# Kernel tuning notes

Hardware: AMD Instinct MI355X
Metric: run time of the kernel (lower is better)

Reference implementation:

```python
import jax, jax.numpy as jnp
import numpy as np

DELTA = 2.5749
BN_EPS = 1e-5
N_LAYERS = 5


def _gin_pna_conv(x, src, dst, nW1, nb1, nW2, nb2, mW, mb):
    # x: [N, D]; src/dst: [E]
    N = x.shape[0]
    msgs = x[src]                                   # [E, D] gather (message = x_j)
    cnt = jax.ops.segment_sum(jnp.ones_like(dst, dtype=x.dtype), dst, num_segments=N)  # [N]
    c = jnp.maximum(cnt, 1.0)[:, None]              # guard isolated nodes
    sums = jax.ops.segment_sum(msgs, dst, num_segments=N)          # [N, D]
    maxs = jax.ops.segment_max(msgs, dst, num_segments=N)
    maxs = jnp.where(cnt[:, None] > 0, maxs, 0.0)   # empty segments -> 0 (torch_scatter behavior)
    means = sums / c
    sq_means = jax.ops.segment_sum(msgs * msgs, dst, num_segments=N) / c
    var = jax.nn.relu(sq_means - means * means)
    base = jnp.concatenate([sums, maxs, means, var], axis=1)        # [N, 4D]
    amp = (c / DELTA) * base                        # amplification scaler
    att = (DELTA / c) * base                        # attenuation scaler
    comb = jnp.concatenate([base, amp, att], axis=1)                # [N, 12D]
    agg = comb @ mW.T + mb                          # mlp: 12D -> D
    h = agg + x                                     # GIN: (1+eps)*x_r + aggr, eps=0
    h = jax.nn.relu(h @ nW1.T + nb1) @ nW2.T + nb2  # nn = Linear-ReLU-Linear
    return h


def _batchnorm(x, gamma, beta):
    mu = jnp.mean(x, axis=0)
    var = jnp.var(x, axis=0)
    return (x - mu) * jax.lax.rsqrt(var + BN_EPS) * gamma + beta


def setup_inputs() -> dict:
    key = jax.random.key(0)
    ks = jax.random.split(key, 12)
    N, E, D, G, OUT = 100000, 1600000, 64, 512, 16
    s = 0.05
    p = lambda k, shape: jax.random.normal(k, shape, dtype=jnp.float32) * s
    return {
        "x": jax.random.normal(ks[0], (N, D), dtype=jnp.float32),
        "edge_index": jax.random.randint(ks[1], (2, E), 0, N),
        "batch": jnp.sort(jax.random.randint(ks[2], (N,), 0, G)),
        "encW": p(ks[3], (D, D)), "encb": jnp.zeros((D,), jnp.float32),
        "nnW1": p(ks[4], (N_LAYERS, D, D)), "nnb1": jnp.zeros((N_LAYERS, D), jnp.float32),
        "nnW2": p(ks[5], (N_LAYERS, D, D)), "nnb2": jnp.zeros((N_LAYERS, D), jnp.float32),
        "mlpW": p(ks[6], (N_LAYERS, D, 12 * D)), "mlpb": jnp.zeros((N_LAYERS, D), jnp.float32),
        "bnG": jnp.ones((N_LAYERS, D), jnp.float32), "bnB": jnp.zeros((N_LAYERS, D), jnp.float32),
        "fc1W": p(ks[7], (D, D)), "fc1b": jnp.zeros((D,), jnp.float32),
        "fc2W": p(ks[8], (OUT, D)), "fc2b": jnp.zeros((OUT,), jnp.float32),
    }


def reference(x, edge_index, batch, encW, encb, nnW1, nnb1, nnW2, nnb2,
              mlpW, mlpb, bnG, bnB, fc1W, fc1b, fc2W, fc2b):
    NUM_GRAPHS = 512
    src, dst = edge_index[0], edge_index[1]
    h = x @ encW.T + encb                           # encoder
    for i in range(N_LAYERS):                       # fixed small layer loop
        h = jax.nn.relu(_gin_pna_conv(h, src, dst, nnW1[i], nnb1[i],
                                      nnW2[i], nnb2[i], mlpW[i], mlpb[i]))
        h = _batchnorm(h, bnG[i], bnB[i])
    g = jax.ops.segment_sum(h, batch, num_segments=NUM_GRAPHS)      # global_add_pool
    g = jax.nn.relu(g @ fc1W.T + fc1b)              # dropout is identity in eval mode
    return g @ fc2W.T + fc2b
```

## Files before the change

### kernel.cpp

```cpp
#include <hip/hip_runtime.h>
#include <hip/hip_bf16.h>
#include <hip/hip_fp16.h>

#define DELTA 2.5749f
#define BN_EPS 1e-5f

#define NBUCK 512
#define NBLK 128
#define ECAP 3584

typedef __attribute__((ext_vector_type(8))) _Float16 f16x8;
typedef __attribute__((ext_vector_type(2))) _Float16 f16x2;
typedef __attribute__((ext_vector_type(4))) float f32x4;

__device__ inline unsigned short f2h(float f) {
    union { _Float16 h; unsigned short u; } v;
    v.h = (_Float16)f;
    return v.u;
}


__global__ __launch_bounds__(256) void k_cnt(const int* __restrict__ dst,
                                             int* __restrict__ cnts,
                                             int E, int npb, int CS) {
    __shared__ int hist[NBUCK];
    int t = threadIdx.x;
    hist[t] = 0; hist[t + 256] = 0;
    __syncthreads();
    int s0 = blockIdx.x * CS, s1 = min(s0 + CS, E);
    for (int e = s0 + t; e < s1; e += 256)
        atomicAdd(&hist[dst[e] / npb], 1);
    __syncthreads();
    cnts[blockIdx.x * NBUCK + t] = hist[t];
    cnts[blockIdx.x * NBUCK + t + 256] = hist[t + 256];
}

__global__ void k_bscan1(const int* __restrict__ cnts, int* __restrict__ bases,
                         int* __restrict__ btot) {
    __shared__ int s[NBLK];
    int b = blockIdx.x, t = threadIdx.x;
    int v = cnts[t * NBUCK + b];
    s[t] = v; __syncthreads();
    for (int off = 1; off < NBLK; off <<= 1) {
        int x = (t >= off) ? s[t - off] : 0;
        __syncthreads();
        s[t] += x;
        __syncthreads();
    }
    bases[t * NBUCK + b] = s[t] - v;
    if (t == NBLK - 1) btot[b] = s[t];
}

__global__ void k_btops(const int* __restrict__ btot, int* __restrict__ bbase,
                        int* __restrict__ rowptr, int E, int N) {
    __shared__ int s[NBUCK];
    int t = threadIdx.x;
    int v = btot[t];
    s[t] = v; __syncthreads();
    for (int off = 1; off < NBUCK; off <<= 1) {
        int x = (t >= off) ? s[t - off] : 0;
        __syncthreads();
        s[t] += x;
        __syncthreads();
    }
    bbase[t] = s[t] - v;
    if (t == 0) rowptr[N] = E;
}

__global__ __launch_bounds__(256) void k_scat(const int* __restrict__ dst,
                                              const int* __restrict__ src,
                                              const int* __restrict__ bases,
                                              const int* __restrict__ bbase,
                                              int* __restrict__ eD,
                                              int* __restrict__ eS,
                                              int E, int npb, int CS) {
    __shared__ int cur[NBUCK];
    int t = threadIdx.x;
    cur[t] = bbase[t] + bases[blockIdx.x * NBUCK + t];
    cur[t + 256] = bbase[t + 256] + bases[blockIdx.x * NBUCK + t + 256];
    __syncthreads();
    int s0 = blockIdx.x * CS, s1 = min(s0 + CS, E);
    for (int e = s0 + t; e < s1; e += 256) {
        int d = dst[e];
        int p = d / npb;
        int pos = atomicAdd(&cur[p], 1);
        eD[pos] = d;
        eS[pos] = src[e];
    }
}

__global__ __launch_bounds__(256) void k_csr(const int* __restrict__ eD,
                                             const int* __restrict__ eS,
                                             const int* __restrict__ bbase,
                                             const int* __restrict__ btot,
                                             int* __restrict__ rowptr,
                                             int* __restrict__ col,
                                             float* __restrict__ cnt,
                                             int npb, int N) {
    __shared__ int sD[ECAP], sS[ECAP];
    __shared__ int pre[256], sc[256];
    int b = blockIdx.x, t = threadIdx.x;
    int lo = b * npb;
    if (lo >= N) return;
    int nn = min(npb, N - lo);
    int base = bbase[b], n = btot[b];
    pre[t] = 0;
    __syncthreads();
    const int* gD = eD + base;
    const int* gS = eS + base;
    for (int i = t; i < n; i += 256) {
        int d = gD[i];
        if (i < ECAP) { sD[i] = d; sS[i] = gS[i]; }
        atomicAdd(&pre[d - lo], 1);
    }
    __syncthreads();
    int deg = (t < nn) ? pre[t] : 0;
    sc[t] = deg; __syncthreads();
    for (int off = 1; off < 256; off <<= 1) {
        int x = (t >= off) ? sc[t - off] : 0;
        __syncthreads();
        sc[t] += x;
        __syncthreads();
    }
    int excl = sc[t] - deg;
    if (t < nn) {
        rowptr[lo + t] = base + excl;
        cnt[lo + t] = (float)(deg > 0 ? deg : 1);
    }
    __syncthreads();
    pre[t] = excl;
    __syncthreads();
    for (int i = t; i < n; i += 256) {
        int d = (i < ECAP) ? sD[i] : gD[i];
        int s = (i < ECAP) ? sS[i] : gS[i];
        int pos = atomicAdd(&pre[d - lo], 1);
        col[base + pos] = s;
    }
}

__global__ void k_castw(const float* __restrict__ w, unsigned short* __restrict__ o, int n4) {
    int i = blockIdx.x * 256 + threadIdx.x;
    if (i < n4) {
        float4 v = ((const float4*)w)[i];
        ushort4 r;
        r.x = f2h(v.x); r.y = f2h(v.y); r.z = f2h(v.z); r.w = f2h(v.w);
        ((ushort4*)o)[i] = r;
    }
}

#define ACC2(V)                                                            \
    do {                                                                   \
        mx = __builtin_elementwise_max(mx, V);                             \
        float x0 = (float)V[0], x1 = (float)V[1];                          \
        sa += x0; qa = fmaf(x0, x0, qa);                                   \
        sb += x1; qb = fmaf(x1, x1, qb);                                   \
    } while (0)

__global__ __launch_bounds__(256) void k_agg(const unsigned short* __restrict__ h16,
                                             const int* __restrict__ rowptr,
                                             const int* __restrict__ col,
                                             const float* __restrict__ bnstat,
                                             const float* __restrict__ gamma,
                                             const float* __restrict__ beta,
                                             float invN, int first,
                                             unsigned short* __restrict__ baseF,
                                             int N) {
    int t = threadIdx.x;
    int lane = t & 63;
    int half = lane >> 5;
    int fl = lane & 31;
    int node = blockIdx.x * 8 + (t >> 6) * 2 + half;
    if (node >= N) return;
    int fo2 = fl * 2;
    float scx, scy, shx, shy;
    if (first) {
        scx = 1.f; scy = 1.f; shx = 0.f; shy = 0.f;
    } else {
        float mu0 = bnstat[fo2] * invN, mu1 = bnstat[fo2 + 1] * invN;
        float v0 = bnstat[64 + fo2] * invN - mu0 * mu0;
        float v1 = bnstat[64 + fo2 + 1] * invN - mu1 * mu1;
        scx = rsqrtf(v0 + BN_EPS) * gamma[fo2];
        scy = rsqrtf(v1 + BN_EPS) * gamma[fo2 + 1];
        shx = beta[fo2] - mu0 * scx;
        shy = beta[fo2 + 1] - mu1 * scy;
    }
    const _Float16* hp = (const _Float16*)h16;
    int s0 = rowptr[node], s1 = rowptr[node + 1];
    int deg = s1 - s0;
    float sa = 0.f, sb = 0.f, qa = 0.f, qb = 0.f;
    f16x2 mx;
    mx[0] = (_Float16)(-65504.0f); mx[1] = (_Float16)(-65504.0f);
    const _Float16* hb = hp + fo2;
    int nfull = deg >> 3;

    f16x2 vA[8];
    int cN[8];
    if (nfull >= 1) {
        int cC[8];
        const int* cp = col + s0;
#pragma unroll
        for (int j = 0; j < 8; j++) cC[j] = cp[j];
        if (nfull >= 2) {
#pragma unroll
            for (int j = 0; j < 8; j++) cN[j] = cp[8 + j];
        }
#pragma unroll
        for (int j = 0; j < 8; j++) vA[j] = *(const f16x2*)(hb + ((size_t)(unsigned)cC[j] << 6));
    }
    for (int b = 1; b < nfull; b++) {
        int cNN[8];
        f16x2 vB[8];
        if (b + 1 < nfull) {
            const int* cp = col + s0 + (b + 1) * 8;
#pragma unroll
            for (int j = 0; j < 8; j++) cNN[j] = cp[j];
        }
#pragma unroll
        for (int j = 0; j < 8; j++) vB[j] = *(const f16x2*)(hb + ((size_t)(unsigned)cN[j] << 6));
#pragma unroll
        for (int j = 0; j < 8; j++) ACC2(vA[j]);
#pragma unroll
        for (int j = 0; j < 8; j++) { vA[j] = vB[j]; }
#pragma unroll
        for (int j = 0; j < 8; j++) { cN[j] = cNN[j]; }
    }
    if (nfull >= 1) {
#pragma unroll
        for (int j = 0; j < 8; j++) ACC2(vA[j]);
    }
    int tb = s0 + nfull * 8;
    int rem = s1 - tb;
    if (rem > 0) {
        int cT[8];
        f16x2 vT[8];
#pragma unroll
        for (int j = 0; j < 8; j++) {
            int idx = (tb + j < s1) ? (tb + j) : (s1 - 1);
            cT[j] = col[idx];
        }
#pragma unroll
        for (int j = 0; j < 8; j++) vT[j] = *(const f16x2*)(hb + ((size_t)(unsigned)cT[j] << 6));
#pragma unroll
        for (int j = 0; j < 8; j++) {
            if (j < rem) ACC2(vT[j]);
        }
    }

    float c = (float)(deg > 0 ? deg : 1);
    float ic = 1.f / c;
    float sum0, sum1, max0, max1, mean0, mean1, var0, var1;
    if (deg == 0) {
        sum0 = sum1 = max0 = max1 = mean0 = mean1 = var0 = var1 = 0.f;
    } else {
        sum0 = fmaf(scx, sa, c * shx);
        sum1 = fmaf(scy, sb, c * shy);
        max0 = fmaf(scx, (float)mx[0], shx);
        max1 = fmaf(scy, (float)mx[1], shy);
        float m0 = sa * ic, m1 = sb * ic;
        mean0 = fmaf(scx, m0, shx);
        mean1 = fmaf(scy, m1, shy);
        var0 = scx * scx * fmaxf(fmaf(-m0, m0, qa * ic), 0.f);
        var1 = scy * scy * fmaxf(fmaf(-m1, m1, qb * ic), 0.f);
    }
    size_t b = (size_t)node * 256 + fo2;
    ushort2 o;
    o.x = f2h(sum0); o.y = f2h(sum1);  *(ushort2*)(baseF + b) = o;
    o.x = f2h(max0); o.y = f2h(max1);  *(ushort2*)(baseF + b + 64) = o;
    o.x = f2h(mean0); o.y = f2h(mean1); *(ushort2*)(baseF + b + 128) = o;
    o.x = f2h(var0); o.y = f2h(var1);  *(ushort2*)(baseF + b + 192) = o;
}

__global__ __launch_bounds__(256) void k_mlp(const unsigned short* __restrict__ baseF,
                                             const float* __restrict__ cnt,
                                             const unsigned short* __restrict__ mWF,
                                             const float* __restrict__ mb,
                                             const unsigned short* __restrict__ hres16,
                                             const float* __restrict__ bnstatPrev,
                                             const float* __restrict__ gammaP,
                                             const float* __restrict__ betaP,
                                             float invN, int first,
                                             const unsigned short* __restrict__ w1F,
                                             const float* __restrict__ b1,
                                             const unsigned short* __restrict__ w2F,
                                             const float* __restrict__ b2,
                                             float* __restrict__ bnstat,
                                             unsigned short* __restrict__ hOut16, int N) {
    __shared__ char smem[49152];
    _Float16* ldsW = (_Float16*)smem;
    _Float16* bufA = (_Float16*)(smem + 12288);
    _Float16* bufB = bufA + 128 * 72;
    float* red = (float*)smem;

    int t = threadIdx.x;
    int wave = t >> 6, lane = t & 63;
    int r16 = lane & 15, quad = lane >> 4;
    int n0 = blockIdx.x * 128;
    int m0 = n0 + wave * 32;

    const _Float16* aptr0 = (const _Float16*)baseF + (size_t)(m0 + r16) * 256 + quad * 8;
    const _Float16* aptr1 = aptr0 + 16 * 256;
    f32x4 acc0[12], acc1[12];
#pragma unroll
    for (int i = 0; i < 12; i++) {
        acc0[i] = (f32x4){0.f, 0.f, 0.f, 0.f};
        acc1[i] = (f32x4){0.f, 0.f, 0.f, 0.f};
    }
    f16x8 aC0 = *(const f16x8*)(aptr0);
    f16x8 aC1 = *(const f16x8*)(aptr1);

#pragma unroll 1
    for (int sc = 0; sc < 8; sc++) {
        if (sc) __syncthreads();
#pragma unroll
        for (int j = 0; j < 3; j++) {
            int rec = wave * 3 + j;
            int mat = rec >> 2, nt = rec & 3;
            uint4 v = *(const uint4*)(mWF + (size_t)(nt * 16 + r16) * 768 + mat * 256
                                      + sc * 32 + quad * 8);
            *(uint4*)((unsigned short*)ldsW + rec * 512 + lane * 8) = v;
        }
        __syncthreads();
        f16x8 aN0, aN1;
        if (sc < 7) {
            aN0 = *(const f16x8*)(aptr0 + (sc + 1) * 32);
            aN1 = *(const f16x8*)(aptr1 + (sc + 1) * 32);
        }
#pragma unroll
        for (int tile = 0; tile < 12; tile++) {
            f16x8 wF = *(const f16x8*)(ldsW + tile * 512 + lane * 8);
            acc0[tile] = __builtin_amdgcn_mfma_f32_16x16x32_f16(aC0, wF, acc0[tile], 0, 0, 0);
            acc1[tile] = __builtin_amdgcn_mfma_f32_16x16x32_f16(aC1, wF, acc1[tile], 0, 0, 0);
        }
        aC0 = aN0; aC1 = aN1;
    }
    __syncthreads();

    {
        int nl = t >> 1, fo = (t & 1) * 32;
        int gn = n0 + nl;
        uint4* dp = (uint4*)(bufA + nl * 72 + fo);
        if (gn < N) {
            const uint4* sp = (const uint4*)(hres16 + (size_t)gn * 64 + fo);
            dp[0] = sp[0]; dp[1] = sp[1]; dp[2] = sp[2]; dp[3] = sp[3];
        } else {
            uint4 z = make_uint4(0, 0, 0, 0);
            dp[0] = z; dp[1] = z; dp[2] = z; dp[3] = z;
        }
    }
    __syncthreads();

    float scf[4], shf[4], mbv[4];
#pragma unroll
    for (int nt = 0; nt < 4; nt++) {
        int f = nt * 16 + r16;
        mbv[nt] = mb[f];
        if (first) {
            scf[nt] = 1.f; shf[nt] = 0.f;
        } else {
            float mu = bnstatPrev[f] * invN;
            float var = bnstatPrev[64 + f] * invN - mu * mu;
            float s = rsqrtf(var + BN_EPS) * gammaP[f];
            scf[nt] = s; shf[nt] = betaP[f] - mu * s;
        }
    }
#pragma unroll
    for (int mt = 0; mt < 2; mt++) {
#pragma unroll
        for (int i = 0; i < 4; i++) {
            int nl = wave * 32 + mt * 16 + quad * 4 + i;
            int gn = n0 + nl;
            if (gn < N) {
                float c = cnt[gn];
                float amp = c / DELTA, att = DELTA / c;
                f32x4* a = mt ? acc1 : acc0;
#pragma unroll
                for (int nt = 0; nt < 4; nt++) {
                    int f = nt * 16 + r16;
                    float r = (float)bufA[nl * 72 + f];
                    float v = a[nt][i] + amp * a[4 + nt][i] + att * a[8 + nt][i]
                            + mbv[nt] + fmaf(r, scf[nt], shf[nt]);
                    bufA[nl * 72 + f] = (_Float16)v;
                }
            }
        }
    }
    __syncthreads();

    f32x4 accN[8];
#pragma unroll
    for (int i = 0; i < 8; i++) accN[i] = (f32x4){0.f, 0.f, 0.f, 0.f};
#pragma unroll
    for (int s = 0; s < 2; s++) {
        f16x8 fA0 = *(const f16x8*)(bufA + (wave * 32 + r16) * 72 + s * 32 + quad * 8);
        f16x8 fA1 = *(const f16x8*)(bufA + (wave * 32 + 16 + r16) * 72 + s * 32 + quad * 8);
#pragma unroll
        for (int nt = 0; nt < 4; nt++) {
            f16x8 wB = *(const f16x8*)((const _Float16*)w1F + (size_t)(nt * 16 + r16) * 64
                                       + s * 32 + quad * 8);
            accN[nt]     = __builtin_amdgcn_mfma_f32_16x16x32_f16(fA0, wB, accN[nt], 0, 0, 0);
            accN[4 + nt] = __builtin_amdgcn_mfma_f32_16x16x32_f16(fA1, wB, accN[4 + nt], 0, 0, 0);
        }
    }
    float b1v[4];
#pragma unroll
    for (int nt = 0; nt < 4; nt++) b1v[nt] = b1[nt * 16 + r16];
#pragma unroll
    for (int mt = 0; mt < 2; mt++) {
#pragma unroll
        for (int i = 0; i < 4; i++) {
            int nl = wave * 32 + mt * 16 + quad * 4 + i;
#pragma unroll
            for (int nt = 0; nt < 4; nt++) {
                float v = fmaxf(accN[mt * 4 + nt][i] + b1v[nt], 0.f);
                bufB[nl * 72 + nt * 16 + r16] = (_Float16)v;
            }
        }
    }
    __syncthreads();

    f32x4 accM[8];
#pragma unroll
    for (int i = 0; i < 8; i++) accM[i] = (f32x4){0.f, 0.f, 0.f, 0.f};
#pragma unroll
    for (int s = 0; s < 2; s++) {
        f16x8 fA0 = *(const f16x8*)(bufB + (wave * 32 + r16) * 72 + s * 32 + quad * 8);
        f16x8 fA1 = *(const f16x8*)(bufB + (wave * 32 + 16 + r16) * 72 + s * 32 + quad * 8);
#pragma unroll
        for (int nt = 0; nt < 4; nt++) {
            f16x8 wB = *(const f16x8*)((const _Float16*)w2F + (size_t)(nt * 16 + r16) * 64
                                       + s * 32 + quad * 8);
            accM[nt]     = __builtin_amdgcn_mfma_f32_16x16x32_f16(fA0, wB, accM[nt], 0, 0, 0);
            accM[4 + nt] = __builtin_amdgcn_mfma_f32_16x16x32_f16(fA1, wB, accM[4 + nt], 0, 0, 0);
        }
    }
    float b2v[4], s1[4], s2[4];
#pragma unroll
    for (int nt = 0; nt < 4; nt++) {
        b2v[nt] = b2[nt * 16 + r16]; s1[nt] = 0.f; s2[nt] = 0.f;
    }
#pragma unroll
    for (int mt = 0; mt < 2; mt++) {
#pragma unroll
        for (int i = 0; i < 4; i++) {
            int nl = wave * 32 + mt * 16 + quad * 4 + i;
            bool ok = (n0 + nl) < N;
#pragma unroll
            for (int nt = 0; nt < 4; nt++) {
                float v = fmaxf(accM[mt * 4 + nt][i] + b2v[nt], 0.f);
                if (ok) { s1[nt] += v; s2[nt] = fmaf(v, v, s2[nt]); }
                bufA[nl * 72 + nt * 16 + r16] = (_Float16)v;
            }
        }
    }
#pragma unroll
    for (int nt = 0; nt < 4; nt++) {
        int row = wave * 4 + quad;
        red[row * 64 + nt * 16 + r16] = s1[nt];
        red[1024 + row * 64 + nt * 16 + r16] = s2[nt];
    }
    __syncthreads();

    {
        int nl = t >> 1, fo = (t & 1) * 32;
        int gn = n0 + nl;
        if (gn < N) {
            const uint4* sp = (const uint4*)(bufA + nl * 72 + fo);
            uint4* dp = (uint4*)(hOut16 + (size_t)gn * 64 + fo);
            dp[0] = sp[0]; dp[1] = sp[1]; dp[2] = sp[2]; dp[3] = sp[3];
        }
    }
    if (t < 128) {
        int d = t & 63, part = t >> 6;
        float tot = 0.f;
#pragma unroll
        for (int r = 0; r < 16; r++) tot += red[part * 1024 + r * 64 + d];
        atomicAdd(&bnstat[part * 64 + d], tot);
    }
}

#define FMA16(ACC0, ACC1, ACC2, ACC3, A, W)                                \
    do {                                                                   \
        ACC0.x = fmaf(A.x, W.x, ACC0.x); ACC0.y = fmaf(A.x, W.y, ACC0.y);  \
        ACC0.z = fmaf(A.x, W.z, ACC0.z); ACC0.w = fmaf(A.x, W.w, ACC0.w);  \
        ACC1.x = fmaf(A.y, W.x, ACC1.x); ACC1.y = fmaf(A.y, W.y, ACC1.y);  \
        ACC1.z = fmaf(A.y, W.z, ACC1.z); ACC1.w = fmaf(A.y, W.w, ACC1.w);  \
        ACC2.x = fmaf(A.z, W.x, ACC2.x); ACC2.y = fmaf(A.z, W.y, ACC2.y);  \
        ACC2.z = fmaf(A.z, W.z, ACC2.z); ACC2.w = fmaf(A.z, W.w, ACC2.w);  \
        ACC3.x = fmaf(A.w, W.x, ACC3.x); ACC3.y = fmaf(A.w, W.y, ACC3.y);  \
        ACC3.z = fmaf(A.w, W.z, ACC3.z); ACC3.w = fmaf(A.w, W.w, ACC3.w);  \
    } while (0)

__global__ __launch_bounds__(256) void k_gemm64(const float* __restrict__ in,
                                                const float* __restrict__ W,
                                                const float* __restrict__ bias,
                                                unsigned short* __restrict__ out16, int N) {
    __shared__ float sInT[64][64];
    __shared__ float sWT[64][64];
    int t = threadIdx.x;
    int tx = t & 15, ty = t >> 4;
    int n0 = blockIdx.x * 64;
    int c4 = tx * 4;
#pragma unroll
    for (int ch = 0; ch < 4; ch++) {
        int row = ch * 16 + ty;
        float4 v = make_float4(0.f, 0.f, 0.f, 0.f);
        if (n0 + row < N) v = *(const float4*)(in + (size_t)(n0 + row) * 64 + c4);
        sInT[c4 + 0][row] = v.x; sInT[c4 + 1][row] = v.y;
        sInT[c4 + 2][row] = v.z; sInT[c4 + 3][row] = v.w;
        float4 w = *(const float4*)(W + (size_t)row * 64 + c4);
        sWT[c4 + 0][row] = w.x; sWT[c4 + 1][row] = w.y;
        sWT[c4 + 2][row] = w.z; sWT[c4 + 3][row] = w.w;
    }
    __syncthreads();
    float4 acc0 = make_float4(0.f, 0.f, 0.f, 0.f);
    float4 acc1 = acc0, acc2 = acc0, acc3 = acc0;
#pragma unroll 8
    for (int k = 0; k < 64; k++) {
        float4 a = *(const float4*)(&sInT[k][ty * 4]);
        float4 w = *(const float4*)(&sWT[k][tx * 4]);
        FMA16(acc0, acc1, acc2, acc3, a, w);
    }
    float4 b4 = *(const float4*)(bias + tx * 4);
#pragma unroll
    for (int i = 0; i < 4; i++) {
        int n = n0 + ty * 4 + i;
        if (n < N) {
            float4 v = (i == 0) ? acc0 : (i == 1) ? acc1 : (i == 2) ? acc2 : acc3;
            v.x += b4.x; v.y += b4.y; v.z += b4.z; v.w += b4.w;
            ushort4 o;
            o.x = f2h(v.x); o.y = f2h(v.y); o.z = f2h(v.z); o.w = f2h(v.w);
            *(ushort4*)(out16 + (size_t)n * 64 + tx * 4) = o;
        }
    }
}

__global__ void k_pool(const unsigned short* __restrict__ h16, const int* __restrict__ batch,
                       const float* __restrict__ bnstat, const float* __restrict__ gamma,
                       const float* __restrict__ beta, float invN,
                       float* __restrict__ g, int N) {
    int d = threadIdx.x & 63, r = threadIdx.x >> 6;
    float mu = bnstat[d] * invN;
    float var = bnstat[64 + d] * invN - mu * mu;
    float sc = rsqrtf(var + BN_EPS) * gamma[d];
    float sh = beta[d] - mu * sc;
    const _Float16* hp = (const _Float16*)h16;
    int nbase = blockIdx.x * 32;
    float acc = 0.f;
    int gcur = -1;
    for (int i = 0; i < 8; i++) {
        int n = nbase + i * 4 + r;
        if (n < N) {
            int gb = batch[n];
            if (gb != gcur) {
                if (gcur >= 0) atomicAdd(&g[gcur * 64 + d], acc);
                acc = 0.f; gcur = gb;
            }
            acc += fmaf((float)hp[(size_t)n * 64 + d], sc, sh);
        }
    }
    if (gcur >= 0) atomicAdd(&g[gcur * 64 + d], acc);
}

__global__ void k_head(const float* __restrict__ g, const float* __restrict__ fc1W,
                       const float* __restrict__ fc1b, const float* __restrict__ fc2W,
                       const float* __restrict__ fc2b, float* __restrict__ out) {
    __shared__ float sg[64], sg1[64];
    int gi = blockIdx.x, t = threadIdx.x;
    sg[t] = g[gi * 64 + t];
    __syncthreads();
    float a = fc1b[t];
    for (int k = 0; k < 64; k++) a = fmaf(sg[k], fc1W[t * 64 + k], a);
    sg1[t] = fmaxf(a, 0.f);
    __syncthreads();
    if (t < 16) {
        float o = fc2b[t];
        for (int k = 0; k < 64; k++) o = fmaf(sg1[k], fc2W[t * 64 + k], o);
        out[gi * 16 + t] = o;
    }
}

extern "C" void kernel_launch(void* const* d_in, const int* in_sizes, int n_in,
                              void* d_out, int out_size, void* d_ws, size_t ws_size,
                              hipStream_t stream) {
    const float* x       = (const float*)d_in[0];
    const int*   eidx    = (const int*)d_in[1];
    const int*   batch   = (const int*)d_in[2];
    const float* encW    = (const float*)d_in[3];
    const float* encb    = (const float*)d_in[4];
    const float* nnW1    = (const float*)d_in[5];
    const float* nnb1    = (const float*)d_in[6];
    const float* nnW2    = (const float*)d_in[7];
    const float* nnb2    = (const float*)d_in[8];
    const float* mlpW    = (const float*)d_in[9];
    const float* mlpb    = (const float*)d_in[10];
    const float* bnG     = (const float*)d_in[11];
    const float* bnB     = (const float*)d_in[12];
    const float* fc1W    = (const float*)d_in[13];
    const float* fc1b    = (const float*)d_in[14];
    const float* fc2W    = (const float*)d_in[15];
    const float* fc2b    = (const float*)d_in[16];
    float* out = (float*)d_out;

    const int N = in_sizes[0] / 64;
    const int E = in_sizes[1] / 2;
    const int G = 512;
    const int* src = eidx;
    const int* dst = eidx + E;
    const int npb = (N + NBUCK - 1) / NBUCK;
    const float invN = 1.f / (float)N;
    const int CS = (E + NBLK - 1) / NBLK;

    char* ws = (char*)d_ws;
    size_t off = 0;
    auto alloc = [&](size_t bytes) { size_t r = off; off = (off + bytes + 255) & ~(size_t)255; return r; };
    int*   rowptr  = (int*)(ws + alloc((size_t)(N + 1) * 4));
    int*   col     = (int*)(ws + alloc((size_t)E * 4));
    int*   eD      = (int*)(ws + alloc((size_t)E * 4));
    int*   eS      = (int*)(ws + alloc((size_t)E * 4));
    int*   cnts    = (int*)(ws + alloc((size_t)NBLK * NBUCK * 4));
    int*   bases   = (int*)(ws + alloc((size_t)NBLK * NBUCK * 4));
    int*   btot    = (int*)(ws + alloc(NBUCK * 4));
    int*   bbase   = (int*)(ws + alloc(NBUCK * 4));
    float* cnt     = (float*)(ws + alloc((size_t)N * 4));
    unsigned short* baseF = (unsigned short*)(ws + alloc((size_t)N * 256 * 2 + 131072));
    unsigned short* hC16 = (unsigned short*)(ws + alloc((size_t)N * 64 * 2 + 32768));
    unsigned short* mWF  = (unsigned short*)(ws + alloc((size_t)5 * 64 * 768 * 2));
    unsigned short* nW1F = (unsigned short*)(ws + alloc((size_t)5 * 64 * 64 * 2));
    unsigned short* nW2F = (unsigned short*)(ws + alloc((size_t)5 * 64 * 64 * 2));
    float* bnstats = (float*)(ws + alloc(5 * 128 * 4));
    float* gpool   = (float*)(ws + alloc((size_t)G * 64 * 4));

    hipMemsetAsync(bnstats, 0, 5 * 128 * 4, stream);
    hipMemsetAsync(gpool, 0, (size_t)G * 64 * 4, stream);

    int ngrid64 = (N + 63) / 64;
    int ngrid128 = (N + 127) / 128;

    k_cnt<<<NBLK, 256, 0, stream>>>(dst, cnts, E, npb, CS);
    k_bscan1<<<NBUCK, NBLK, 0, stream>>>(cnts, bases, btot);
    k_btops<<<1, NBUCK, 0, stream>>>(btot, bbase, rowptr, E, N);
    k_scat<<<NBLK, 256, 0, stream>>>(dst, src, bases, bbase, eD, eS, E, npb, CS);
    k_csr<<<NBUCK, 256, 0, stream>>>(eD, eS, bbase, btot, rowptr, col, cnt, npb, N);

    k_castw<<<240, 256, 0, stream>>>(mlpW, mWF, 61440);
    k_castw<<<20, 256, 0, stream>>>(nnW1, nW1F, 5120);
    k_castw<<<20, 256, 0, stream>>>(nnW2, nW2F, 5120);

    k_gemm64<<<ngrid64, 256, 0, stream>>>(x, encW, encb, hC16, N);

    for (int i = 0; i < 5; i++) {
        const float* bsPrev = (i == 0) ? bnstats : bnstats + (i - 1) * 128;
        const float* gP = (i == 0) ? bnG : bnG + (i - 1) * 64;
        const float* bP = (i == 0) ? bnB : bnB + (i - 1) * 64;
        int first = (i == 0) ? 1 : 0;
        k_agg<<<(N + 7) / 8, 256, 0, stream>>>(hC16, rowptr, col, bsPrev, gP, bP,
                                               invN, first, baseF, N);
        k_mlp<<<ngrid128, 256, 0, stream>>>(baseF, cnt,
                                            mWF + (size_t)i * 64 * 768, mlpb + i * 64,
                                            hC16, bsPrev, gP, bP, invN, first,
                                            nW1F + (size_t)i * 4096, nnb1 + i * 64,
                                            nW2F + (size_t)i * 4096, nnb2 + i * 64,
                                            bnstats + i * 128, hC16, N);
    }

    k_pool<<<(N + 31) / 32, 256, 0, stream>>>(hC16, batch, bnstats + 4 * 128,
                                              bnG + 4 * 64, bnB + 4 * 64, invN, gpool, N);
    k_head<<<G, 64, 0, stream>>>(gpool, fc1W, fc1b, fc2W, fc2b, out);
}
```

Before: 676.6 us.

## Pack edge pairs as int2 and read MLP weights directly from global

The edge bucket scatter now writes interleaved (dst,src) int2 pairs, so the CSR build does one 8-byte load per edge instead of two separate 4-byte loads. In the main MLP kernel, the per-chunk staging of mlp weights through LDS and its two barriers are removed. Each wave now loads its MFMA B-operands straight from global memory, which shrinks LDS to 36 KB and may raise occupancy. The cost is redundant global/L2 weight traffic across waves, and a barrier is moved later to protect the reuse of the shared buffers.

```diff
diff --git a/kernel.cpp b/kernel.cpp
--- a/kernel.cpp
+++ b/kernel.cpp
@@ -71,8 +71,7 @@
                                               const int* __restrict__ src,
                                               const int* __restrict__ bases,
                                               const int* __restrict__ bbase,
-                                              int* __restrict__ eD,
-                                              int* __restrict__ eS,
+                                              int2* __restrict__ eDS,
                                               int E, int npb, int CS) {
     __shared__ int cur[NBUCK];
     int t = threadIdx.x;
@@ -84,20 +83,18 @@
         int d = dst[e];
         int p = d / npb;
         int pos = atomicAdd(&cur[p], 1);
-        eD[pos] = d;
-        eS[pos] = src[e];
-    }
-}
-
-__global__ __launch_bounds__(256) void k_csr(const int* __restrict__ eD,
-                                             const int* __restrict__ eS,
+        eDS[pos] = make_int2(d, src[e]);
+    }
+}
+
+__global__ __launch_bounds__(256) void k_csr(const int2* __restrict__ eDS,
                                              const int* __restrict__ bbase,
                                              const int* __restrict__ btot,
                                              int* __restrict__ rowptr,
                                              int* __restrict__ col,
                                              float* __restrict__ cnt,
                                              int npb, int N) {
-    __shared__ int sD[ECAP], sS[ECAP];
+    __shared__ int2 sE[ECAP];
     __shared__ int pre[256], sc[256];
     int b = blockIdx.x, t = threadIdx.x;
     int lo = b * npb;
@@ -106,12 +103,11 @@
     int base = bbase[b], n = btot[b];
     pre[t] = 0;
     __syncthreads();
-    const int* gD = eD + base;
-    const int* gS = eS + base;
+    const int2* gE = eDS + base;
     for (int i = t; i < n; i += 256) {
-        int d = gD[i];
-        if (i < ECAP) { sD[i] = d; sS[i] = gS[i]; }
-        atomicAdd(&pre[d - lo], 1);
+        int2 e = gE[i];
+        if (i < ECAP) sE[i] = e;
+        atomicAdd(&pre[e.x - lo], 1);
     }
     __syncthreads();
     int deg = (t < nn) ? pre[t] : 0;
@@ -131,10 +127,9 @@
     pre[t] = excl;
     __syncthreads();
     for (int i = t; i < n; i += 256) {
-        int d = (i < ECAP) ? sD[i] : gD[i];
-        int s = (i < ECAP) ? sS[i] : gS[i];
-        int pos = atomicAdd(&pre[d - lo], 1);
-        col[base + pos] = s;
+        int2 e = (i < ECAP) ? sE[i] : gE[i];
+        int pos = atomicAdd(&pre[e.x - lo], 1);
+        col[base + pos] = e.y;
     }
 }
 
@@ -285,11 +280,10 @@
                                              const float* __restrict__ b2,
                                              float* __restrict__ bnstat,
                                              unsigned short* __restrict__ hOut16, int N) {
-    __shared__ char smem[49152];
-    _Float16* ldsW = (_Float16*)smem;
-    _Float16* bufA = (_Float16*)(smem + 12288);
+    __shared__ char smem[36864];
+    _Float16* bufA = (_Float16*)smem;
     _Float16* bufB = bufA + 128 * 72;
-    float* red = (float*)smem;
+    float* red = (float*)bufB;
 
     int t = threadIdx.x;
     int wave = t >> 6, lane = t & 63;
@@ -299,6 +293,7 @@
 
     const _Float16* aptr0 = (const _Float16*)baseF + (size_t)(m0 + r16) * 256 + quad * 8;
     const _Float16* aptr1 = aptr0 + 16 * 256;
+    const _Float16* mW = (const _Float16*)mWF;
     f32x4 acc0[12], acc1[12];
 #pragma unroll
     for (int i = 0; i < 12; i++) {
@@ -310,16 +305,6 @@
 
 #pragma unroll 1
     for (int sc = 0; sc < 8; sc++) {
-        if (sc) __syncthreads();
-#pragma unroll
-        for (int j = 0; j < 3; j++) {
-            int rec = wave * 3 + j;
-            int mat = rec >> 2, nt = rec & 3;
-            uint4 v = *(const uint4*)(mWF + (size_t)(nt * 16 + r16) * 768 + mat * 256
-                                      + sc * 32 + quad * 8);
-            *(uint4*)((unsigned short*)ldsW + rec * 512 + lane * 8) = v;
-        }
-        __syncthreads();
         f16x8 aN0, aN1;
         if (sc < 7) {
             aN0 = *(const f16x8*)(aptr0 + (sc + 1) * 32);
@@ -327,13 +312,14 @@
         }
 #pragma unroll
         for (int tile = 0; tile < 12; tile++) {
-            f16x8 wF = *(const f16x8*)(ldsW + tile * 512 + lane * 8);
-            acc0[tile] = __builtin_amdgcn_mfma_f32_16x16x32_f16(aC0, wF, acc0[tile], 0, 0, 0);
-            acc1[tile] = __builtin_amdgcn_mfma_f32_16x16x32_f16(aC1, wF, acc1[tile], 0, 0, 0);
+            int mat = tile >> 2, nt = tile & 3;
+            f16x8 wB = *(const f16x8*)(mW + (size_t)(nt * 16 + r16) * 768 + mat * 256
+                                       + sc * 32 + quad * 8);
+            acc0[tile] = __builtin_amdgcn_mfma_f32_16x16x32_f16(aC0, wB, acc0[tile], 0, 0, 0);
+            acc1[tile] = __builtin_amdgcn_mfma_f32_16x16x32_f16(aC1, wB, acc1[tile], 0, 0, 0);
         }
         aC0 = aN0; aC1 = aN1;
     }
-    __syncthreads();
 
     {
         int nl = t >> 1, fo = (t & 1) * 32;
@@ -433,6 +419,7 @@
             accM[4 + nt] = __builtin_amdgcn_mfma_f32_16x16x32_f16(fA1, wB, accM[4 + nt], 0, 0, 0);
         }
     }
+    __syncthreads();
     float b2v[4], s1[4], s2[4];
 #pragma unroll
     for (int nt = 0; nt < 4; nt++) {
@@ -615,8 +602,7 @@
     auto alloc = [&](size_t bytes) { size_t r = off; off = (off + bytes + 255) & ~(size_t)255; return r; };
     int*   rowptr  = (int*)(ws + alloc((size_t)(N + 1) * 4));
     int*   col     = (int*)(ws + alloc((size_t)E * 4));
-    int*   eD      = (int*)(ws + alloc((size_t)E * 4));
-    int*   eS      = (int*)(ws + alloc((size_t)E * 4));
+    int2*  eDS     = (int2*)(ws + alloc((size_t)E * 8));
     int*   cnts    = (int*)(ws + alloc((size_t)NBLK * NBUCK * 4));
     int*   bases   = (int*)(ws + alloc((size_t)NBLK * NBUCK * 4));
     int*   btot    = (int*)(ws + alloc(NBUCK * 4));
@@ -639,8 +625,8 @@
     k_cnt<<<NBLK, 256, 0, stream>>>(dst, cnts, E, npb, CS);
     k_bscan1<<<NBUCK, NBLK, 0, stream>>>(cnts, bases, btot);
     k_btops<<<1, NBUCK, 0, stream>>>(btot, bbase, rowptr, E, N);
-    k_scat<<<NBLK, 256, 0, stream>>>(dst, src, bases, bbase, eD, eS, E, npb, CS);
-    k_csr<<<NBUCK, 256, 0, stream>>>(eD, eS, bbase, btot, rowptr, col, cnt, npb, N);
+    k_scat<<<NBLK, 256, 0, stream>>>(dst, src, bases, bbase, eDS, E, npb, CS);
+    k_csr<<<NBUCK, 256, 0, stream>>>(eDS, bbase, btot, rowptr, col, cnt, npb, N);
 
     k_castw<<<240, 256, 0, stream>>>(mlpW, mWF, 61440);
     k_castw<<<20, 256, 0, stream>>>(nnW1, nW1F, 5120);
```

Result: slower. 815.4 us (+20.5%).
